# Kernel tuning notes

Hardware: AMD Instinct MI355X
Metric: run time of the kernel (lower is better)

Reference implementation:

```python
import jax, jax.numpy as jnp
import numpy as np
import math

B, S, DIM = 2, 2048, 2048
H, KVH, HD = 32, 8, 64          # n_heads, n_kv_heads, head_dim = dim // n_heads
N_REP = H // KVH                # 4
ROPE_THETA = 10000.0


def _apply_rotary(x, cos, sin):
    # x: [B, S, nh, HD]; cos/sin: [S, HD//2]
    # pairs (x[..., 2i], x[..., 2i+1]) treated as complex a+ib, multiplied by cos+isin
    xr = x.reshape(*x.shape[:-1], HD // 2, 2)
    a, b = xr[..., 0], xr[..., 1]
    c = cos[None, :, None, :]
    s = sin[None, :, None, :]
    out = jnp.stack([a * c - b * s, a * s + b * c], axis=-1)
    return out.reshape(x.shape)


def setup_inputs() -> dict:
    key = jax.random.key(0)
    ks = jax.random.split(key, 5)
    x = jax.random.normal(ks[0], (B, S, DIM), dtype=jnp.float32)
    scale = 1.0 / math.sqrt(DIM)
    wq = jax.random.normal(ks[1], (DIM, H * HD), dtype=jnp.float32) * scale
    wk = jax.random.normal(ks[2], (DIM, KVH * HD), dtype=jnp.float32) * scale
    wv = jax.random.normal(ks[3], (DIM, KVH * HD), dtype=jnp.float32) * scale
    wo = jax.random.normal(ks[4], (H * HD, DIM), dtype=jnp.float32) * scale
    # RoPE frequencies: freqs_cis = exp(i * t * theta^{-2k/HD}), k = 0..HD/2-1
    inv_freq = 1.0 / (ROPE_THETA ** (jnp.arange(0, HD, 2, dtype=jnp.float32) / HD))
    angles = jnp.arange(S, dtype=jnp.float32)[:, None] * inv_freq[None, :]  # [S, HD//2]
    freqs_cos = jnp.cos(angles)
    freqs_sin = jnp.sin(angles)
    # causal mask: True = masked out
    mask = jnp.triu(jnp.ones((1, 1, S, S), dtype=bool), k=1)
    return {"x": x, "wq": wq, "wk": wk, "wv": wv, "wo": wo,
            "freqs_cos": freqs_cos, "freqs_sin": freqs_sin,
            "mask": mask, "start_pos": 0}


def reference(x, wq, wk, wv, wo, freqs_cos, freqs_sin, mask, start_pos):
    del start_pos  # unused, matching original
    bsz, seqlen, _ = x.shape
    xq = (x @ wq).reshape(bsz, seqlen, H, HD)
    xk = (x @ wk).reshape(bsz, seqlen, KVH, HD)
    xv = (x @ wv).reshape(bsz, seqlen, KVH, HD)
    xq = _apply_rotary(xq, freqs_cos, freqs_sin)
    xk = _apply_rotary(xk, freqs_cos, freqs_sin)
    # repeat_kv: [B,S,KVH,HD] -> [B,S,H,HD]
    xk = jnp.repeat(xk[:, :, :, None, :], N_REP, axis=3).reshape(bsz, seqlen, H, HD)
    xv = jnp.repeat(xv[:, :, :, None, :], N_REP, axis=3).reshape(bsz, seqlen, H, HD)
    xq = jnp.transpose(xq, (0, 2, 1, 3))  # [B,H,S,HD]
    xk = jnp.transpose(xk, (0, 2, 1, 3))
    xv = jnp.transpose(xv, (0, 2, 1, 3))
    scores = jnp.einsum('bhqd,bhkd->bhqk', xq, xk) / math.sqrt(HD)
    scores = jnp.where(mask, -jnp.inf, scores)
    probs = jax.nn.softmax(scores.astype(jnp.float32), axis=-1).astype(xq.dtype)
    out = jnp.einsum('bhqk,bhkd->bhqd', probs, xv)
    out = jnp.transpose(out, (0, 2, 1, 3)).reshape(bsz, seqlen, H * HD)
    return out @ wo
```

## Files before the change

kernel.cpp:

```cpp
#include <hip/hip_runtime.h>


using u16   = unsigned short;
using u32   = unsigned int;
using f32x4 = __attribute__((ext_vector_type(4))) float;
using f32x16= __attribute__((ext_vector_type(16))) float;
using s16x8 = __attribute__((ext_vector_type(8))) short;
using b16x8 = __attribute__((ext_vector_type(8))) __bf16;
using u16x4 = __attribute__((ext_vector_type(4))) unsigned short;
using u32x4 = __attribute__((ext_vector_type(4))) u32;

__device__ __forceinline__ u16 f2bf(float f) {
  u32 u = __builtin_bit_cast(u32, f);
  u = (u + 0x7fffu + ((u >> 16) & 1u)) >> 16;
  return (u16)u;
}
__device__ __forceinline__ float bf2f(u32 lo16) {
  return __builtin_bit_cast(float, lo16 << 16);
}

__device__ __forceinline__ f32x4 mfma16(s16x8 a, s16x8 b, f32x4 c) {
  return __builtin_amdgcn_mfma_f32_16x16x32_bf16(
      __builtin_bit_cast(b16x8, a), __builtin_bit_cast(b16x8, b), c, 0, 0, 0);
}
__device__ __forceinline__ f32x16 mfma32(s16x8 a, s16x8 b, f32x16 c) {
  return __builtin_amdgcn_mfma_f32_32x32x16_bf16(
      __builtin_bit_cast(b16x8, a), __builtin_bit_cast(b16x8, b), c, 0, 0, 0);
}

__device__ __forceinline__ void gload_lds16(const void* g, void* l) {
  __builtin_amdgcn_global_load_lds(
      (const __attribute__((address_space(1))) void*)g,
      (__attribute__((address_space(3))) void*)l, 16, 0, 0);
}

__device__ __forceinline__ u32 cvtpk(float lo, float hi) {
  u32 r; asm("v_cvt_pk_bf16_f32 %0, %1, %2" : "=v"(r) : "v"(lo), "v"(hi));
  return r;
}

__device__ __forceinline__ float fexp2(float x) {
#if __has_builtin(__builtin_amdgcn_exp2f)
  return __builtin_amdgcn_exp2f(x);
#else
  return exp2f(x);
#endif
}

__global__ __launch_bounds__(256) void cvt_kernel(const float* __restrict__ src,
                                                  u16* __restrict__ dst, int n4) {
  int i = blockIdx.x * 256 + threadIdx.x;
  if (i >= n4) return;
  f32x4 v = *(const f32x4*)(src + (size_t)i * 4);
  u16x4 r;
#pragma unroll
  for (int j = 0; j < 4; ++j) r[j] = f2bf(v[j]);
  *(u16x4*)(dst + (size_t)i * 4) = r;
}

__global__ __launch_bounds__(256) void tcvt_kernel(const float* __restrict__ src,
                                                   u16* __restrict__ dst, int N) {
  __shared__ float t[32][33];
  const int n0 = blockIdx.x * 32, k0 = blockIdx.y * 32;
  const int tx = threadIdx.x & 31, ty = threadIdx.x >> 5;
#pragma unroll
  for (int r = 0; r < 4; ++r)
    t[ty + 8 * r][tx] = src[(size_t)(k0 + ty + 8 * r) * N + n0 + tx];
  __syncthreads();
#pragma unroll
  for (int r = 0; r < 4; ++r)
    dst[(size_t)(n0 + ty + 8 * r) * 2048 + k0 + tx] = f2bf(t[tx][ty + 8 * r]);
}

__global__ __launch_bounds__(256) void rope_kernel(u16* __restrict__ qkv,
                                                   const float* __restrict__ cs,
                                                   const float* __restrict__ sn) {
  const int m = blockIdx.x;
  const int p = blockIdx.y * 256 + threadIdx.x;
  const int s = m & 2047;
  int col, d2;
  if (p < 1024) { col = 2 * p; d2 = p & 31; }
  else { int pk = p - 1024; col = 2048 + 2 * pk; d2 = pk & 31; }
  const float c = cs[s * 32 + d2], si = sn[s * 32 + d2];
  u32* addr = (u32*)&qkv[(size_t)m * 3072 + col];
  u32 v = *addr;
  float a = bf2f(v & 0xffffu), b = bf2f(v >> 16);
  float na = a * c - b * si;
  float nb = a * si + b * c;
  *addr = (u32)f2bf(na) | ((u32)f2bf(nb) << 16);
}

__global__ __launch_bounds__(256) void vt_kernel(const u16* __restrict__ qkv,
                                                 u16* __restrict__ VtG) {
  __shared__ u16 t[64][65];
  const int s0 = blockIdx.x * 64;
  const int bk = blockIdx.y;
  const int b = bk >> 3, kvh = bk & 7;
  const int tx = threadIdx.x & 63, ty = threadIdx.x >> 6;
#pragma unroll
  for (int r = 0; r < 16; ++r)
    t[ty + 4 * r][tx] =
        qkv[(size_t)(b * 2048 + s0 + ty + 4 * r) * 3072 + 2560 + kvh * 64 + tx];
  __syncthreads();
#pragma unroll
  for (int r = 0; r < 16; ++r)
    VtG[(size_t)(bk * 64 + ty + 4 * r) * 2048 + s0 + tx] = t[tx][ty + 4 * r];
}

template <bool BF16OUT>
__global__ __launch_bounds__(256) void gemm_bt(const u16* __restrict__ A,
                                               const u16* __restrict__ Bt,
                                               void* __restrict__ Cv,
                                               int M, int N, int K, int GX) {
  __shared__ u16 As[2][128 * 32];
  __shared__ u16 Bs[2][128 * 32];
  const int tid = threadIdx.x;
  const int wid = tid >> 6, lane = tid & 63;
  const int l15 = lane & 15, lq = lane >> 4;
  const int wr = wid >> 1, wc = wid & 1;
  const int cpx = gridDim.x >> 3;
  const int swz = (blockIdx.x & 7) * cpx + (blockIdx.x >> 3);
  const int m0 = (swz / GX) * 128, n0 = (swz % GX) * 128;

  const int srow16 = lane >> 2;
  const int k8 = (lane & 3) * 8;

  auto STAGE = [&](int bb, int kt) {
#pragma unroll
    for (int i = 0; i < 2; ++i) {
      const int r = wid * 2 + i;
      const int row = r * 16 + srow16;
      gload_lds16(A + (size_t)(m0 + row) * K + kt + k8, &As[bb][r * 512]);
      gload_lds16(Bt + (size_t)(n0 + row) * K + kt + k8, &Bs[bb][r * 512]);
    }
  };

  f32x4 acc[4][4] = {};
  STAGE(0, 0);
  __syncthreads();
  int cur = 0;
  for (int kt = 0; kt < K; kt += 32) {
    if (kt + 32 < K) STAGE(cur ^ 1, kt + 32);
    s16x8 af[4], bf[4];
#pragma unroll
    for (int i = 0; i < 4; ++i)
      af[i] = *(const s16x8*)&As[cur][(wr * 64 + i * 16 + l15) * 32 + 8 * lq];
#pragma unroll
    for (int j = 0; j < 4; ++j)
      bf[j] = *(const s16x8*)&Bs[cur][(wc * 64 + j * 16 + l15) * 32 + 8 * lq];
#pragma unroll
    for (int i = 0; i < 4; ++i)
#pragma unroll
      for (int j = 0; j < 4; ++j)
        acc[i][j] = mfma16(af[i], bf[j], acc[i][j]);
    __syncthreads();
    cur ^= 1;
  }

  u16* Cb = (u16*)Cv;
  float* Cf = (float*)Cv;
#pragma unroll
  for (int i = 0; i < 4; ++i)
#pragma unroll
    for (int j = 0; j < 4; ++j)
#pragma unroll
      for (int r = 0; r < 4; ++r) {
        const int row = m0 + wr * 64 + i * 16 + 4 * lq + r;
        const int col = n0 + wc * 64 + j * 16 + l15;
        if constexpr (BF16OUT) Cb[(size_t)row * N + col] = f2bf(acc[i][j][r]);
        else                   Cf[(size_t)row * N + col] = acc[i][j][r];
      }
}

__global__ __launch_bounds__(256) void attn_kernel(const u16* __restrict__ qkv,
                                                   const u16* __restrict__ VtG,
                                                   u16* __restrict__ aout) {
  constexpr int QSTR = 3072;
  constexpr float SCL = 0.18033688011112042f;
  const int bx = blockIdx.x;
  const int bh = blockIdx.y;
  const int b = bh >> 5, h = bh & 31, kvh = h >> 2;
  const int tid = threadIdx.x, w = tid >> 6;
  const int l31 = tid & 31, hh = (tid >> 5) & 1;

  __shared__ u16 Ks[4][64 * 64];
  __shared__ u16 Vs[4][64 * 64];

  const int srow = tid >> 3, sslot = tid & 7;
  const int sd8 = (sslot ^ (srow & 7)) * 8;
  const u16* kg = qkv + (size_t)(b * 2048 + srow) * QSTR + 2048 + kvh * 64 + sd8;
  const u16* vg = VtG + (size_t)((b * 8 + kvh) * 64 + srow) * 2048 + sd8;
  const int xsw = l31 & 7;

  auto STAGE = [&](int bb, int t) {
    const size_t ko = (size_t)t * 64 * QSTR;
    const size_t vo = (size_t)t * 64;
    gload_lds16(kg + ko, &Ks[bb][w * 512]);
    gload_lds16(kg + ko + (size_t)32 * QSTR, &Ks[bb][2048 + w * 512]);
    gload_lds16(vg + vo, &Vs[bb][w * 512]);
    gload_lds16(vg + vo + (size_t)32 * 2048, &Vs[bb][2048 + w * 512]);
  };

  auto process = [&](int qt) {
    const int q_abs = qt * 128 + w * 32 + l31;
    const u16* qrow = qkv + (size_t)(b * 2048 + q_abs) * QSTR + h * 64;
    s16x8 qf[4];
#pragma unroll
    for (int s = 0; s < 4; ++s) qf[s] = *(const s16x8*)(qrow + 16 * s + 8 * hh);

    f32x16 o0 = {}, o1 = {};
    float mrun = 0.f, lrun = 0.f;

    const int nt = 2 * qt + 2;
    STAGE(0, 0);
    STAGE(1, 1);

    for (int t = 0; t < nt; ++t) {
      if (t + 2 < nt) {
        STAGE((t + 2) & 3, t + 2);
        asm volatile("s_waitcnt vmcnt(8)" ::: "memory");
      } else if (t + 2 == nt) {
        asm volatile("s_waitcnt vmcnt(4)" ::: "memory");
      } else {
        asm volatile("s_waitcnt vmcnt(0)" ::: "memory");
      }
      __builtin_amdgcn_s_barrier();

      const int kv0 = t * 64;
      if (kv0 <= qt * 128 + w * 32 + 31) {
        const u16* Kb = &Ks[t & 3][0];
        const u16* Vb = &Vs[t & 3][0];

        f32x16 a0 = {}, a1 = {};
        __builtin_amdgcn_s_setprio(1);
#pragma unroll
        for (int s = 0; s < 4; ++s) {
          const int c0 = ((2 * s + hh) ^ xsw) * 8;
          s16x8 k0 = *(const s16x8*)(Kb + l31 * 64 + c0);
          s16x8 k1 = *(const s16x8*)(Kb + (32 + l31) * 64 + c0);
          a0 = mfma32(k0, qf[s], a0);
          a1 = mfma32(k1, qf[s], a1);
        }
        __builtin_amdgcn_s_setprio(0);

        if (kv0 + 63 > qt * 128 + w * 32) {
#pragma unroll
          for (int r = 0; r < 16; ++r) {
            const int kva = kv0 + (r & 3) + 8 * (r >> 2) + 4 * hh;
            if (kva > q_abs) a0[r] = -3e38f;
            if (kva + 32 > q_abs) a1[r] = -3e38f;
          }
        }

        float mxr = -3e38f;
#pragma unroll
        for (int r = 0; r < 16; ++r) mxr = fmaxf(mxr, fmaxf(a0[r], a1[r]));
        float mx = fmaxf(mxr * SCL, __shfl_xor(mxr * SCL, 32));
        const bool need = __any(mx > mrun + 8.f);
        float mnew = mrun, c1 = 1.f;
        if (need) {
          mnew = fmaxf(mrun, mx);
          c1 = fexp2(mrun - mnew);
        }

        float sum = 0.f;
#pragma unroll
        for (int r = 0; r < 16; ++r) {
          a0[r] = fexp2(__builtin_fmaf(a0[r], SCL, -mnew));
          a1[r] = fexp2(__builtin_fmaf(a1[r], SCL, -mnew));
          sum += a0[r] + a1[r];
        }
        sum += __shfl_xor(sum, 32);
        lrun = lrun * c1 + sum;
        mrun = mnew;
        if (need) {
#pragma unroll
          for (int r = 0; r < 16; ++r) { o0[r] *= c1; o1[r] *= c1; }
        }

        s16x8 pf[4];
#pragma unroll
        for (int s = 0; s < 4; ++s) {
          const f32x16& ps = (s & 2) ? a1 : a0;
          const int g4 = (s & 1) * 8;
          u32 x  = cvtpk(ps[g4 + 0], ps[g4 + 1]);
          u32 x2 = cvtpk(ps[g4 + 2], ps[g4 + 3]);
          u32 y  = cvtpk(ps[g4 + 4], ps[g4 + 5]);
          u32 y2 = cvtpk(ps[g4 + 6], ps[g4 + 7]);
          asm("v_permlane32_swap_b32 %0, %1" : "+v"(x), "+v"(y));
          asm("v_permlane32_swap_b32 %0, %1" : "+v"(x2), "+v"(y2));
          u32x4 fr = {x, x2, y, y2};
          pf[s] = __builtin_bit_cast(s16x8, fr);
        }

        __builtin_amdgcn_s_setprio(1);
#pragma unroll
        for (int s = 0; s < 4; ++s) {
          const int c0 = ((2 * s + hh) ^ xsw) * 8;
          s16x8 v0f = *(const s16x8*)(Vb + l31 * 64 + c0);
          s16x8 v1f = *(const s16x8*)(Vb + (32 + l31) * 64 + c0);
          o0 = mfma32(v0f, pf[s], o0);
          o1 = mfma32(v1f, pf[s], o1);
        }
        __builtin_amdgcn_s_setprio(0);
      }
    }
    __syncthreads();

    const float inv = 1.f / lrun;
    u16* ob = aout + (size_t)(b * 2048 + q_abs) * 2048 + h * 64;
#pragma unroll
    for (int g = 0; g < 4; ++g) {
      u16x4 w0, w1;
#pragma unroll
      for (int j = 0; j < 4; ++j) {
        w0[j] = f2bf(o0[4 * g + j] * inv);
        w1[j] = f2bf(o1[4 * g + j] * inv);
      }
      *(u16x4*)(ob + 8 * g + 4 * hh) = w0;
      *(u16x4*)(ob + 32 + 8 * g + 4 * hh) = w1;
    }
  };

  process(15 - bx);
  process(bx);
}

extern "C" void kernel_launch(void* const* d_in, const int* in_sizes, int n_in,
                              void* d_out, int out_size, void* d_ws, size_t ws_size,
                              hipStream_t stream) {
  const float* x    = (const float*)d_in[0];
  const float* wq   = (const float*)d_in[1];
  const float* wk   = (const float*)d_in[2];
  const float* wv   = (const float*)d_in[3];
  const float* wo   = (const float*)d_in[4];
  const float* cosT = (const float*)d_in[5];
  const float* sinT = (const float*)d_in[6];
  float* out = (float*)d_out;

  const size_t SZ_XB   = (size_t)4096 * 2048 * 2;
  const size_t SZ_WQKV = (size_t)3072 * 2048 * 2;
  const size_t SZ_WO   = (size_t)2048 * 2048 * 2;
  const size_t SZ_QKV  = (size_t)4096 * 3072 * 2;
  const size_t SZ_ATT  = (size_t)4096 * 2048 * 2;
  if (ws_size < SZ_XB + SZ_WQKV + SZ_WO + SZ_QKV + SZ_ATT) return;

  char* p = (char*)d_ws;
  u16* xb    = (u16*)p; p += SZ_XB;
  u16* wqkvT = (u16*)p; p += SZ_WQKV;
  u16* woT   = (u16*)p; p += SZ_WO;
  u16* qkv   = (u16*)p; p += SZ_QKV;
  u16* attn  = (u16*)p; p += SZ_ATT;
  u16* VtG   = xb;

  cvt_kernel<<<8192, 256, 0, stream>>>(x, xb, 2097152);
  tcvt_kernel<<<dim3(64, 64), 256, 0, stream>>>(wq, wqkvT, 2048);
  tcvt_kernel<<<dim3(16, 64), 256, 0, stream>>>(wk, wqkvT + (size_t)2048 * 2048, 512);
  tcvt_kernel<<<dim3(16, 64), 256, 0, stream>>>(wv, wqkvT + (size_t)2560 * 2048, 512);
  tcvt_kernel<<<dim3(64, 64), 256, 0, stream>>>(wo, woT, 2048);

  gemm_bt<true><<<768, 256, 0, stream>>>(xb, wqkvT, qkv, 4096, 3072, 2048, 24);
  rope_kernel<<<dim3(4096, 5), 256, 0, stream>>>(qkv, cosT, sinT);
  vt_kernel<<<dim3(32, 16), 256, 0, stream>>>(qkv, VtG);
  attn_kernel<<<dim3(8, 64), 256, 0, stream>>>(qkv, VtG, attn);
  gemm_bt<false><<<512, 256, 0, stream>>>(attn, woT, out, 4096, 2048, 2048, 16);
}
```

Measured before the change: 222.9 us.

## Process paired high and low query tiles in one shared KV stream

Instead of running two sequential passes (high query tile then low query tile), each reloading K/V tiles, the block now streams K/V once and computes both query tiles against each staged tile where causally needed. This removes the duplicate K/V loads for the low tile and one full pipeline prologue/epilogue, at the cost of doubled accumulator and Q-fragment registers, which may reduce occupancy or cause spills. The row max and sum reductions are also rewritten as tree reductions, and the online-softmax rescale now folds lrun scaling into the conditional branch.

```diff
diff --git a/kernel.cpp b/kernel.cpp
--- a/kernel.cpp
+++ b/kernel.cpp
@@ -201,129 +201,147 @@
     gload_lds16(vg + vo + (size_t)32 * 2048, &Vs[bb][2048 + w * 512]);
   };
 
-  auto process = [&](int qt) {
-    const int q_abs = qt * 128 + w * 32 + l31;
-    const u16* qrow = qkv + (size_t)(b * 2048 + q_abs) * QSTR + h * 64;
-    s16x8 qf[4];
-#pragma unroll
-    for (int s = 0; s < 4; ++s) qf[s] = *(const s16x8*)(qrow + 16 * s + 8 * hh);
-
-    f32x16 o0 = {}, o1 = {};
-    float mrun = 0.f, lrun = 0.f;
-
-    const int nt = 2 * qt + 2;
-    STAGE(0, 0);
-    STAGE(1, 1);
-
-    for (int t = 0; t < nt; ++t) {
-      if (t + 2 < nt) {
-        STAGE((t + 2) & 3, t + 2);
-        asm volatile("s_waitcnt vmcnt(8)" ::: "memory");
-      } else if (t + 2 == nt) {
-        asm volatile("s_waitcnt vmcnt(4)" ::: "memory");
-      } else {
-        asm volatile("s_waitcnt vmcnt(0)" ::: "memory");
+  const int qh = 15 - bx, ql = bx;
+  const int qah = qh * 128 + w * 32 + l31;
+  const int qal = ql * 128 + w * 32 + l31;
+
+  const u16* qrh = qkv + (size_t)(b * 2048 + qah) * QSTR + h * 64;
+  const u16* qrl = qkv + (size_t)(b * 2048 + qal) * QSTR + h * 64;
+  s16x8 qfh[4], qfl[4];
+#pragma unroll
+  for (int s = 0; s < 4; ++s) {
+    qfh[s] = *(const s16x8*)(qrh + 16 * s + 8 * hh);
+    qfl[s] = *(const s16x8*)(qrl + 16 * s + 8 * hh);
+  }
+
+  f32x16 oh0 = {}, oh1 = {}, ol0 = {}, ol1 = {};
+  float mh = 0.f, lh = 0.f, ml = 0.f, ll = 0.f;
+
+  auto tile_compute = [&](const u16* Kb, const u16* Vb, int kv0, int qt,
+                          int q_abs, const s16x8* qf, f32x16& o0, f32x16& o1,
+                          float& mrun, float& lrun) {
+    f32x16 a0 = {}, a1 = {};
+    __builtin_amdgcn_s_setprio(1);
+#pragma unroll
+    for (int s = 0; s < 4; ++s) {
+      const int c0 = ((2 * s + hh) ^ xsw) * 8;
+      s16x8 k0 = *(const s16x8*)(Kb + l31 * 64 + c0);
+      s16x8 k1 = *(const s16x8*)(Kb + (32 + l31) * 64 + c0);
+      a0 = mfma32(k0, qf[s], a0);
+      a1 = mfma32(k1, qf[s], a1);
+    }
+    __builtin_amdgcn_s_setprio(0);
+
+    if (kv0 + 63 > qt * 128 + w * 32) {
+#pragma unroll
+      for (int r = 0; r < 16; ++r) {
+        const int kva = kv0 + (r & 3) + 8 * (r >> 2) + 4 * hh;
+        if (kva > q_abs) a0[r] = -3e38f;
+        if (kva + 32 > q_abs) a1[r] = -3e38f;
       }
-      __builtin_amdgcn_s_barrier();
-
-      const int kv0 = t * 64;
-      if (kv0 <= qt * 128 + w * 32 + 31) {
-        const u16* Kb = &Ks[t & 3][0];
-        const u16* Vb = &Vs[t & 3][0];
-
-        f32x16 a0 = {}, a1 = {};
-        __builtin_amdgcn_s_setprio(1);
-#pragma unroll
-        for (int s = 0; s < 4; ++s) {
-          const int c0 = ((2 * s + hh) ^ xsw) * 8;
-          s16x8 k0 = *(const s16x8*)(Kb + l31 * 64 + c0);
-          s16x8 k1 = *(const s16x8*)(Kb + (32 + l31) * 64 + c0);
-          a0 = mfma32(k0, qf[s], a0);
-          a1 = mfma32(k1, qf[s], a1);
-        }
-        __builtin_amdgcn_s_setprio(0);
-
-        if (kv0 + 63 > qt * 128 + w * 32) {
-#pragma unroll
-          for (int r = 0; r < 16; ++r) {
-            const int kva = kv0 + (r & 3) + 8 * (r >> 2) + 4 * hh;
-            if (kva > q_abs) a0[r] = -3e38f;
-            if (kva + 32 > q_abs) a1[r] = -3e38f;
-          }
-        }
-
-        float mxr = -3e38f;
-#pragma unroll
-        for (int r = 0; r < 16; ++r) mxr = fmaxf(mxr, fmaxf(a0[r], a1[r]));
-        float mx = fmaxf(mxr * SCL, __shfl_xor(mxr * SCL, 32));
-        const bool need = __any(mx > mrun + 8.f);
-        float mnew = mrun, c1 = 1.f;
-        if (need) {
-          mnew = fmaxf(mrun, mx);
-          c1 = fexp2(mrun - mnew);
-        }
-
-        float sum = 0.f;
-#pragma unroll
-        for (int r = 0; r < 16; ++r) {
-          a0[r] = fexp2(__builtin_fmaf(a0[r], SCL, -mnew));
-          a1[r] = fexp2(__builtin_fmaf(a1[r], SCL, -mnew));
-          sum += a0[r] + a1[r];
-        }
-        sum += __shfl_xor(sum, 32);
-        lrun = lrun * c1 + sum;
-        mrun = mnew;
-        if (need) {
-#pragma unroll
-          for (int r = 0; r < 16; ++r) { o0[r] *= c1; o1[r] *= c1; }
-        }
-
-        s16x8 pf[4];
-#pragma unroll
-        for (int s = 0; s < 4; ++s) {
-          const f32x16& ps = (s & 2) ? a1 : a0;
-          const int g4 = (s & 1) * 8;
-          u32 x  = cvtpk(ps[g4 + 0], ps[g4 + 1]);
-          u32 x2 = cvtpk(ps[g4 + 2], ps[g4 + 3]);
-          u32 y  = cvtpk(ps[g4 + 4], ps[g4 + 5]);
-          u32 y2 = cvtpk(ps[g4 + 6], ps[g4 + 7]);
-          asm("v_permlane32_swap_b32 %0, %1" : "+v"(x), "+v"(y));
-          asm("v_permlane32_swap_b32 %0, %1" : "+v"(x2), "+v"(y2));
-          u32x4 fr = {x, x2, y, y2};
-          pf[s] = __builtin_bit_cast(s16x8, fr);
-        }
-
-        __builtin_amdgcn_s_setprio(1);
-#pragma unroll
-        for (int s = 0; s < 4; ++s) {
-          const int c0 = ((2 * s + hh) ^ xsw) * 8;
-          s16x8 v0f = *(const s16x8*)(Vb + l31 * 64 + c0);
-          s16x8 v1f = *(const s16x8*)(Vb + (32 + l31) * 64 + c0);
-          o0 = mfma32(v0f, pf[s], o0);
-          o1 = mfma32(v1f, pf[s], o1);
-        }
-        __builtin_amdgcn_s_setprio(0);
-      }
-    }
-    __syncthreads();
-
-    const float inv = 1.f / lrun;
-    u16* ob = aout + (size_t)(b * 2048 + q_abs) * 2048 + h * 64;
-#pragma unroll
-    for (int g = 0; g < 4; ++g) {
-      u16x4 w0, w1;
-#pragma unroll
-      for (int j = 0; j < 4; ++j) {
-        w0[j] = f2bf(o0[4 * g + j] * inv);
-        w1[j] = f2bf(o1[4 * g + j] * inv);
-      }
-      *(u16x4*)(ob + 8 * g + 4 * hh) = w0;
-      *(u16x4*)(ob + 32 + 8 * g + 4 * hh) = w1;
-    }
+    }
+
+    float mr[16];
+#pragma unroll
+    for (int r = 0; r < 16; ++r) mr[r] = fmaxf(a0[r], a1[r]);
+#pragma unroll
+    for (int s2 = 8; s2 >= 1; s2 >>= 1)
+#pragma unroll
+      for (int r = 0; r < s2; ++r) mr[r] = fmaxf(mr[r], mr[r + s2]);
+    const float mxs = mr[0] * SCL;
+    const float mx = fmaxf(mxs, __shfl_xor(mxs, 32));
+    if (__any(mx > mrun + 8.f)) {
+      const float mnew = fmaxf(mrun, mx);
+      const float c1 = fexp2(mrun - mnew);
+      mrun = mnew;
+      lrun *= c1;
+#pragma unroll
+      for (int r = 0; r < 16; ++r) { o0[r] *= c1; o1[r] *= c1; }
+    }
+
+#pragma unroll
+    for (int r = 0; r < 16; ++r) {
+      a0[r] = fexp2(__builtin_fmaf(a0[r], SCL, -mrun));
+      a1[r] = fexp2(__builtin_fmaf(a1[r], SCL, -mrun));
+    }
+    float sr[16];
+#pragma unroll
+    for (int r = 0; r < 16; ++r) sr[r] = a0[r] + a1[r];
+#pragma unroll
+    for (int s2 = 8; s2 >= 1; s2 >>= 1)
+#pragma unroll
+      for (int r = 0; r < s2; ++r) sr[r] += sr[r + s2];
+    lrun += sr[0] + __shfl_xor(sr[0], 32);
+
+    s16x8 pf[4];
+#pragma unroll
+    for (int s = 0; s < 4; ++s) {
+      const f32x16& ps = (s & 2) ? a1 : a0;
+      const int g4 = (s & 1) * 8;
+      u32 x  = cvtpk(ps[g4 + 0], ps[g4 + 1]);
+      u32 x2 = cvtpk(ps[g4 + 2], ps[g4 + 3]);
+      u32 y  = cvtpk(ps[g4 + 4], ps[g4 + 5]);
+      u32 y2 = cvtpk(ps[g4 + 6], ps[g4 + 7]);
+      asm("v_permlane32_swap_b32 %0, %1" : "+v"(x), "+v"(y));
+      asm("v_permlane32_swap_b32 %0, %1" : "+v"(x2), "+v"(y2));
+      u32x4 fr = {x, x2, y, y2};
+      pf[s] = __builtin_bit_cast(s16x8, fr);
+    }
+
+    __builtin_amdgcn_s_setprio(1);
+#pragma unroll
+    for (int s = 0; s < 4; ++s) {
+      const int c0 = ((2 * s + hh) ^ xsw) * 8;
+      s16x8 v0f = *(const s16x8*)(Vb + l31 * 64 + c0);
+      s16x8 v1f = *(const s16x8*)(Vb + (32 + l31) * 64 + c0);
+      o0 = mfma32(v0f, pf[s], o0);
+      o1 = mfma32(v1f, pf[s], o1);
+    }
+    __builtin_amdgcn_s_setprio(0);
   };
 
-  process(15 - bx);
-  process(bx);
+  const int nth = 2 * qh + 2;
+  STAGE(0, 0);
+  STAGE(1, 1);
+
+  for (int t = 0; t < nth; ++t) {
+    if (t + 2 < nth) {
+      STAGE((t + 2) & 3, t + 2);
+      asm volatile("s_waitcnt vmcnt(8)" ::: "memory");
+    } else if (t + 2 == nth) {
+      asm volatile("s_waitcnt vmcnt(4)" ::: "memory");
+    } else {
+      asm volatile("s_waitcnt vmcnt(0)" ::: "memory");
+    }
+    __builtin_amdgcn_s_barrier();
+
+    const int kv0 = t * 64;
+    const u16* Kb = &Ks[t & 3][0];
+    const u16* Vb = &Vs[t & 3][0];
+    if (kv0 <= qh * 128 + w * 32 + 31)
+      tile_compute(Kb, Vb, kv0, qh, qah, qfh, oh0, oh1, mh, lh);
+    if (kv0 <= ql * 128 + w * 32 + 31)
+      tile_compute(Kb, Vb, kv0, ql, qal, qfl, ol0, ol1, ml, ll);
+  }
+
+  const float invh = 1.f / lh, invl = 1.f / ll;
+  u16* obh = aout + (size_t)(b * 2048 + qah) * 2048 + h * 64;
+  u16* obl = aout + (size_t)(b * 2048 + qal) * 2048 + h * 64;
+#pragma unroll
+  for (int g = 0; g < 4; ++g) {
+    u16x4 w0, w1, w2, w3;
+#pragma unroll
+    for (int j = 0; j < 4; ++j) {
+      w0[j] = f2bf(oh0[4 * g + j] * invh);
+      w1[j] = f2bf(oh1[4 * g + j] * invh);
+      w2[j] = f2bf(ol0[4 * g + j] * invl);
+      w3[j] = f2bf(ol1[4 * g + j] * invl);
+    }
+    *(u16x4*)(obh + 8 * g + 4 * hh) = w0;
+    *(u16x4*)(obh + 32 + 8 * g + 4 * hh) = w1;
+    *(u16x4*)(obl + 8 * g + 4 * hh) = w2;
+    *(u16x4*)(obl + 32 + 8 * g + 4 * hh) = w3;
+  }
 }
 
 extern "C" void kernel_launch(void* const* d_in, const int* in_sizes, int n_in,
```

After: 256.8 us. 15.2% more time.

## Add 256x256-tile 8-wave GEMM kernel for the QKV projection

Applied to the files above, without the earlier changes.

Replaces the 128x128-tile, 4-wave GEMM used for the fused QKV projection with a new 256x256-tile kernel using 512 threads, a 64-deep K step and double-buffered direct global-to-LDS loads. Each wave computes a 128x64 sub-tile in four phases separated by barriers, with raised wave priority around the MFMA bursts. The aim is more operand reuse per LDS byte and fewer global loads per output. The trade-off is only 192 blocks on a GPU with many CUs, so some CUs may sit idle and load balance may suffer; register pressure and LDS use per block also go up.

```diff
diff --git a/kernel.cpp b/kernel.cpp
--- a/kernel.cpp
+++ b/kernel.cpp
@@ -107,6 +107,105 @@
     VtG[(size_t)(bk * 64 + ty + 4 * r) * 2048 + s0 + tx] = t[tx][ty + 4 * r];
 }
 
+__global__ __launch_bounds__(512, 2) void gemm256(const u16* __restrict__ A,
+                                                  const u16* __restrict__ Bt,
+                                                  u16* __restrict__ C,
+                                                  int M, int N, int K, int GX) {
+  __shared__ u16 As[2][16 * 2 * 512];
+  __shared__ u16 Bs[2][16 * 2 * 512];
+  const int tid = threadIdx.x;
+  const int wv = tid >> 6, lane = tid & 63;
+  const int l15 = lane & 15, lq = lane >> 4;
+  const int wm = wv >> 2, wn = wv & 3;
+  const int cpx = gridDim.x >> 3;
+  const int swz = (blockIdx.x & 7) * cpx + (blockIdx.x >> 3);
+  const int m0 = (swz / GX) * 256, n0 = (swz % GX) * 256;
+
+  const int sr = lane & 15, sk = 8 * (lane >> 4);
+
+  auto STAGE = [&](int bb, int kt) {
+#pragma unroll
+    for (int i = 0; i < 4; ++i) {
+      const int fk = wv * 4 + i;
+      const int f = fk >> 1, ks = fk & 1;
+      const size_t gro = (size_t)(f * 16 + sr);
+      const int gk = kt + ks * 32 + sk;
+      gload_lds16(A + (m0 + gro) * K + gk, &As[bb][fk * 512]);
+      gload_lds16(Bt + (n0 + gro) * K + gk, &Bs[bb][fk * 512]);
+    }
+  };
+
+  f32x4 acc[8][4] = {};
+  STAGE(0, 0);
+  __syncthreads();
+  int c = 0;
+
+  for (int kt = 0; kt < K; kt += 64) {
+    s16x8 a4[4], b4[4];
+#pragma unroll
+    for (int i = 0; i < 4; ++i)
+      a4[i] = *(const s16x8*)&As[c][((wm * 8 + i) * 2 + 0) * 512 + lane * 8];
+#pragma unroll
+    for (int j = 0; j < 4; ++j)
+      b4[j] = *(const s16x8*)&Bs[c][((wn * 4 + j) * 2 + 0) * 512 + lane * 8];
+    if (kt + 64 < K) STAGE(c ^ 1, kt + 64);
+    __builtin_amdgcn_s_setprio(1);
+#pragma unroll
+    for (int i = 0; i < 4; ++i)
+#pragma unroll
+      for (int j = 0; j < 4; ++j) acc[i][j] = mfma16(a4[i], b4[j], acc[i][j]);
+    __builtin_amdgcn_s_setprio(0);
+    __builtin_amdgcn_s_barrier();
+#pragma unroll
+    for (int i = 0; i < 4; ++i)
+      a4[i] = *(const s16x8*)&As[c][((wm * 8 + 4 + i) * 2 + 0) * 512 + lane * 8];
+    __builtin_amdgcn_s_setprio(1);
+#pragma unroll
+    for (int i = 0; i < 4; ++i)
+#pragma unroll
+      for (int j = 0; j < 4; ++j)
+        acc[4 + i][j] = mfma16(a4[i], b4[j], acc[4 + i][j]);
+    __builtin_amdgcn_s_setprio(0);
+    __builtin_amdgcn_s_barrier();
+#pragma unroll
+    for (int i = 0; i < 4; ++i)
+      a4[i] = *(const s16x8*)&As[c][((wm * 8 + i) * 2 + 1) * 512 + lane * 8];
+#pragma unroll
+    for (int j = 0; j < 4; ++j)
+      b4[j] = *(const s16x8*)&Bs[c][((wn * 4 + j) * 2 + 1) * 512 + lane * 8];
+    __builtin_amdgcn_s_setprio(1);
+#pragma unroll
+    for (int i = 0; i < 4; ++i)
+#pragma unroll
+      for (int j = 0; j < 4; ++j) acc[i][j] = mfma16(a4[i], b4[j], acc[i][j]);
+    __builtin_amdgcn_s_setprio(0);
+    __builtin_amdgcn_s_barrier();
+#pragma unroll
+    for (int i = 0; i < 4; ++i)
+      a4[i] = *(const s16x8*)&As[c][((wm * 8 + 4 + i) * 2 + 1) * 512 + lane * 8];
+    __builtin_amdgcn_s_setprio(1);
+#pragma unroll
+    for (int i = 0; i < 4; ++i)
+#pragma unroll
+      for (int j = 0; j < 4; ++j)
+        acc[4 + i][j] = mfma16(a4[i], b4[j], acc[4 + i][j]);
+    __builtin_amdgcn_s_setprio(0);
+    __syncthreads();
+    c ^= 1;
+  }
+
+#pragma unroll
+  for (int i = 0; i < 8; ++i)
+#pragma unroll
+    for (int j = 0; j < 4; ++j)
+#pragma unroll
+      for (int r = 0; r < 4; ++r) {
+        const int row = m0 + wm * 128 + i * 16 + 4 * lq + r;
+        const int col = n0 + wn * 64 + j * 16 + l15;
+        C[(size_t)row * N + col] = f2bf(acc[i][j][r]);
+      }
+}
+
 template <bool BF16OUT>
 __global__ __launch_bounds__(256) void gemm_bt(const u16* __restrict__ A,
                                                const u16* __restrict__ Bt,
@@ -359,7 +458,7 @@
   tcvt_kernel<<<dim3(16, 64), 256, 0, stream>>>(wv, wqkvT + (size_t)2560 * 2048, 512);
   tcvt_kernel<<<dim3(64, 64), 256, 0, stream>>>(wo, woT, 2048);
 
-  gemm_bt<true><<<768, 256, 0, stream>>>(xb, wqkvT, qkv, 4096, 3072, 2048, 24);
+  gemm256<<<192, 512, 0, stream>>>(xb, wqkvT, qkv, 4096, 3072, 2048, 12);
   rope_kernel<<<dim3(4096, 5), 256, 0, stream>>>(qkv, cosT, sinT);
   vt_kernel<<<dim3(32, 16), 256, 0, stream>>>(qkv, VtG);
   attn_kernel<<<dim3(8, 64), 256, 0, stream>>>(qkv, VtG, attn);
```

Result: slower. 240.3 us (+7.8%).
